# Kernel optimization log

Hardware: AMD Instinct MI355X
Metric: run time of the kernel (lower is better)

## Reference

```python
import jax, jax.numpy as jnp
import numpy as np

# ---- static physical configuration (matches init_kwargs param dict) ----
NX = NY = 513
NL = 3
N_ENS = 4
LX = LY = 5120.0e3
DX = LX / (NX - 1)
DY = LY / (NY - 1)
F0 = 9.375e-5
BETA = 1.754e-11
A2 = 0.0
A4 = 2.0e9
DELTA_EK = 2.0
TAU0 = 2.0e-5
BCCO = 0.2
ZFBC = BCCO / (1.0 + 0.5 * BCCO)
DT = 600.0
NUM_STEPS = 4
HEIGHTS = np.array([350.0, 750.0, 2900.0])
RED_G = np.array([0.025, 0.0125])

JAC_COEF = 1.0 / (F0 * DX * DY)
HYPERDIFF_COEF = A4 / F0**2 / DX**6
BOTTOM_FRICTION_COEF = DELTA_EK / (2.0 * abs(F0) * DX**2 * (-HEIGHTS[-1]))


def _build_constants():
    """Precompute stratification / mode / Helmholtz matrices (float64 numpy, cast to f32)."""
    A = np.zeros((NL, NL))
    A[0, 0] = 1.0 / (HEIGHTS[0] * RED_G[0])
    A[0, 1] = -1.0 / (HEIGHTS[0] * RED_G[0])
    for i in range(1, NL - 1):
        A[i, i - 1] = -1.0 / (HEIGHTS[i] * RED_G[i - 1])
        A[i, i] = 1.0 / HEIGHTS[i] * (1.0 / RED_G[i] + 1.0 / RED_G[i - 1])
        A[i, i + 1] = -1.0 / (HEIGHTS[i] * RED_G[i])
    A[-1, -1] = 1.0 / (HEIGHTS[NL - 1] * RED_G[NL - 2])
    A[-1, -2] = -1.0 / (HEIGHTS[NL - 1] * RED_G[NL - 2])
    lam_r, R = np.linalg.eig(A)
    lam_l, L = np.linalg.eig(A.T)
    lam_r, R, lam_l, L = lam_r.real, R.real, lam_l.real, L.real
    # align left eigenvectors with right eigenvalue ordering (biorthogonality)
    order = np.array([int(np.argmin(np.abs(lam_l - lr))) for lr in lam_r])
    L = L[:, order]
    Cl2m = np.diag(1.0 / np.diag(L.T @ R)) @ L.T
    Cm2l = R
    lambd = lam_r
    # DST-I eigenvalues of the 5-point Laplacian on the interior grid
    xg, yg = np.meshgrid(np.arange(1, NX - 1), np.arange(1, NY - 1), indexing='ij')
    lap_dst = (2 * (np.cos(np.pi / (NX - 1) * xg) - 1) / DX**2
               + 2 * (np.cos(np.pi / (NY - 1) * yg) - 1) / DY**2)
    helm_dst = lap_dst[None] / F0**2 - lambd[:, None, None]  # (nl, nx-2, ny-2)

    def np_dstI1D(x):
        N = x.shape[-1]
        xp = np.zeros(x.shape[:-1] + (N + 2,))
        xp[..., 1:-1] = x
        return np.fft.irfft(-1j * xp, n=2 * (N + 1), axis=-1, norm='ortho')[..., 1:N + 1]

    def np_dstI2D(x):
        return np.swapaxes(np_dstI1D(np.swapaxes(np_dstI1D(x), -1, -2)), -1, -2)

    const = np.ones((NL, NX, NY)) / (NX * NY)
    s = np.zeros_like(const)
    s[:, 1:-1, 1:-1] = np_dstI2D(np_dstI2D(const[:, 1:-1, 1:-1]) / helm_dst)
    hom_sol = (const + s * lambd[:, None, None])[:-1]  # (nl-1, nx, ny)
    M = (Cm2l[1:] - Cm2l[:-1])[:NL - 1, :NL - 1] * hom_sol.mean((1, 2))[None, :]
    alpha = -np.linalg.inv(M) @ (Cm2l[1:, :-1] - Cm2l[:-1, :-1])
    # wind forcing: curl(tau)/(f0*H1) on interior points; tau_y = 0, tau_x(y) only
    tau_x = -TAU0 * np.cos(2 * np.pi * (np.arange(NY) + 0.5) / NY)[None, :] * np.ones((NX, NY))
    dtaux_dy = (tau_x[1:-1, 2:] - tau_x[1:-1, :-2]) / (2 * DY)
    wind = (-dtaux_dy / (F0 * HEIGHTS[0]))[None]  # (1, nx-2, ny-2)
    f32 = lambda a: jnp.asarray(a, jnp.float32)
    return dict(A=f32(A), Cl2m=f32(Cl2m), Cm2l=f32(Cm2l), helmoltz_dst=f32(helm_dst),
                alpha_matrix=f32(alpha), homogeneous_sol=f32(hom_sol), wind_forcing=f32(wind))


# ---------------- stencil ops ----------------

def _pad11(x):
    return jnp.pad(x, [(0, 0)] * (x.ndim - 2) + [(1, 1), (1, 1)])


def laplacian_h_nobc(f):
    # unscaled 5-point Laplacian, interior values only: (..., nx-2, ny-2)
    return (f[..., 2:, 1:-1] + f[..., :-2, 1:-1] + f[..., 1:-1, 2:] + f[..., 1:-1, :-2]
            - 4.0 * f[..., 1:-1, 1:-1])


def laplacian_h(f, fc):
    # full-grid Laplacian with partial-slip boundary treatment (coefficient fc = zfbc)
    lap = _pad11(laplacian_h_nobc(f))
    lap = lap.at[..., 0, :].set(fc * (f[..., 1, :] - f[..., 0, :]))
    lap = lap.at[..., -1, :].set(fc * (f[..., -2, :] - f[..., -1, :]))
    lap = lap.at[..., :, 0].set(fc * (f[..., :, 1] - f[..., :, 0]))
    lap = lap.at[..., :, -1].set(fc * (f[..., :, -2] - f[..., :, -1]))
    return lap


def laplacian_h_boundaries(f, fc):
    # boundary Laplacian values, concat order: x=0 (y interior), x=-1, y=0 (full x), y=-1
    return jnp.concatenate([
        fc * (f[..., 1, 1:-1] - f[..., 0, 1:-1]),
        fc * (f[..., -2, 1:-1] - f[..., -1, 1:-1]),
        fc * (f[..., :, 1] - f[..., :, 0]),
        fc * (f[..., :, -2] - f[..., :, -1])], axis=-1)


def jacobi_h(f, g):
    # Arakawa 9-point Jacobian J(f, g), interior values (..., nx-2, ny-2)
    dx_f = f[..., 2:, :] - f[..., :-2, :]
    dx_g = g[..., 2:, :] - g[..., :-2, :]
    dy_f = f[..., 2:] - f[..., :-2]
    dy_g = g[..., 2:] - g[..., :-2]
    return ((dx_f[..., 1:-1] * dy_g[..., 1:-1, :] - dx_g[..., 1:-1] * dy_f[..., 1:-1, :])
            + (f[..., 2:, 1:-1] * dy_g[..., 2:, :] - f[..., :-2, 1:-1] * dy_g[..., :-2, :])
            - (f[..., 1:-1, 2:] * dx_g[..., 2:] - f[..., 1:-1, :-2] * dx_g[..., :-2])
            + (g[..., 1:-1, 2:] * dx_f[..., 2:] - g[..., 1:-1, :-2] * dx_f[..., :-2])
            - (g[..., 2:, 1:-1] * dy_f[..., 2:, :] - g[..., :-2, 1:-1] * dy_f[..., :-2, :])) / 12.0


# ---------------- DST-I elliptic solve ----------------

def dstI1D(x):
    N = x.shape[-1]
    z = jnp.zeros(x.shape[:-1] + (1,), x.dtype)
    xp = jnp.concatenate([z, x, z], axis=-1)
    return jnp.fft.irfft(-1j * xp.astype(jnp.complex64), n=2 * (N + 1), axis=-1,
                         norm='ortho')[..., 1:N + 1]


def dstI2D(x):
    return jnp.swapaxes(dstI1D(jnp.swapaxes(dstI1D(x), -1, -2)), -1, -2)


def inverse_elliptic_dst(f, op_dst):
    return dstI2D(dstI2D(f) / op_dst)


# ---------------- QG time derivative ----------------

def _time_derivatives(y, A, Cl2m, Cm2l, helm_dst, alpha, hom_sol, wind):
    q, p = y[0], y[1]  # (..., nl, nx, ny)
    # advection + hyperdiffusion RHS on interior (a_2 == 0 branch skipped as in source)
    rhs = JAC_COEF * jacobi_h(q, p)
    delta2_p = laplacian_h(p, ZFBC)
    rhs = rhs - HYPERDIFF_COEF * laplacian_h_nobc(laplacian_h(delta2_p, ZFBC))
    rhs = rhs.at[..., 0:1, :, :].add(wind)
    rhs = rhs.at[..., -1:, :, :].add(BOTTOM_FRICTION_COEF * laplacian_h_nobc(p[..., -1:, :, :]))
    dq = _pad11(rhs)
    # layers -> modes, DST Helmholtz inversion, homogeneous-solution correction
    rhs_h = jnp.einsum('ij,...jxy->...ixy', Cl2m, dq)
    dp_modes = _pad11(inverse_elliptic_dst(rhs_h[..., 1:-1, 1:-1], helm_dst))
    mean_m = dp_modes[..., :-1, :, :].mean((-2, -1))  # (..., nl-1)
    dalpha = jnp.einsum('ij,...j->...i', alpha, mean_m)[..., None, None]
    dp_modes = dp_modes.at[..., :-1, :, :].add(dalpha * hom_sol)
    dp = jnp.einsum('ij,...jxy->...ixy', Cm2l, dp_modes)
    # boundary vorticity update
    dp_bound = jnp.concatenate([dp[..., 0, 1:-1], dp[..., -1, 1:-1],
                                dp[..., :, 0], dp[..., :, -1]], axis=-1)
    delta_p_bound = laplacian_h_boundaries(dp / (F0 * DX)**2, ZFBC)
    dq_bound = delta_p_bound - jnp.einsum('ij,...jl->...il', A, dp_bound)
    ny2 = NY - 2
    dq = dq.at[..., 0, 1:-1].set(dq_bound[..., :ny2])
    dq = dq.at[..., -1, 1:-1].set(dq_bound[..., ny2:2 * ny2])
    dq = dq.at[..., :, 0].set(dq_bound[..., 2 * ny2:2 * ny2 + NX])
    dq = dq.at[..., :, -1].set(dq_bound[..., 2 * ny2 + NX:2 * ny2 + 2 * NX])
    return jnp.stack((dq, dp), 0)


def _forecast(y0, t, A, Cl2m, Cm2l, helm_dst, alpha, hom_sol, wind):
    deriv = lambda y: _time_derivatives(y, A, Cl2m, Cm2l, helm_dst, alpha, hom_sol, wind)

    def step(y, dt_):
        k1 = deriv(y)
        k2 = deriv(y + 0.5 * dt_ * k1)
        k3 = deriv(y + 0.5 * dt_ * k2)
        k4 = deriv(y + dt_ * k3)
        y_next = y + (dt_ / 6.0) * (k1 + 2.0 * k2 + 2.0 * k3 + k4)
        return y_next, y_next

    _, traj = jax.lax.scan(step, y0, t[1:] - t[:-1])
    return jnp.concatenate([y0[None], traj], axis=0)  # (T, 2, n_ens, nl, nx, ny)


def setup_inputs() -> dict:
    key = jax.random.key(0)
    y0 = 0.1 * jax.random.normal(key, (2, N_ENS, NL, NX, NY), dtype=jnp.float32)
    t = jnp.arange(NUM_STEPS + 1, dtype=jnp.float32) * DT
    consts = _build_constants()
    return dict(y0=y0, t=t, **consts)


def reference(y0, t, A, Cl2m, Cm2l, helmoltz_dst, alpha_matrix, homogeneous_sol, wind_forcing):
    return _forecast(y0, t, A, Cl2m, Cm2l, helmoltz_dst, alpha_matrix,
                     homogeneous_sol, wind_forcing)
```

## Files before the change

### kernel.cpp

```cpp
#include <hip/hip_runtime.h>
#include <math.h>

#define NXY 513
#define NIN 511
#define NL3 3
#define NE4 4
#define NB 12
#define GLD 512

static constexpr long FS  = (long)NE4 * NL3 * NXY * NXY;
static constexpr long GSZ = (long)NB * GLD * GLD;
static constexpr int  NSTEPS = 4;

static constexpr double dF0 = 9.375e-05;
static constexpr double dDX = 10000.0;
static constexpr float ZFBCf     = (float)(0.2 / (1.0 + 0.5 * 0.2));
static constexpr float JACCf     = (float)(1.0 / (dF0 * dDX * dDX));
static constexpr float HYPCf     = (float)(2.0e9 / (dF0 * dF0) / (dDX*dDX*dDX*dDX*dDX*dDX));
static constexpr float BFCf      = (float)(2.0 / (2.0 * dF0 * dDX * dDX * (-2900.0)));
static constexpr float INVF0DX2f = (float)(1.0 / ((dF0 * dDX) * (dF0 * dDX)));

typedef short  bf16x8 __attribute__((ext_vector_type(8)));
typedef float  f32x4  __attribute__((ext_vector_type(4)));
typedef unsigned int u32;
typedef __attribute__((address_space(1))) const u32 GAS;
typedef __attribute__((address_space(3))) u32 LAS;
#define GLDS(gp, lp) __builtin_amdgcn_global_load_lds((GAS*)(gp), (LAS*)(lp), 16, 0, 0)

__device__ __forceinline__ unsigned short f2bf(float x) {
    unsigned int u = __float_as_uint(x);
    return (unsigned short)((u + 0x7FFFu + ((u >> 16) & 1u)) >> 16);
}
__device__ __forceinline__ float bf2f(unsigned short h) {
    return __uint_as_float(((unsigned int)h) << 16);
}

__global__ void initB_kernel(unsigned short* __restrict__ BoH, unsigned short* __restrict__ BoL,
                             unsigned short* __restrict__ BeH, unsigned short* __restrict__ BeL) {
    int j = threadIdx.x;
    int n = blockIdx.x;
    int idx = n * 256 + j;
    int mo = ((n + 1) * (2 * j + 1)) & 1023;
    int me = ((n + 1) * (2 * j + 2)) & 1023;
    float fo = (float)(0.0625 * sin(M_PI * (double)mo / 512.0));
    float fe = (float)(0.0625 * sin(M_PI * (double)me / 512.0));
    unsigned short oh = f2bf(fo);
    BoH[idx] = oh; BoL[idx] = f2bf(fo - bf2f(oh));
    unsigned short eh = f2bf(fe);
    BeH[idx] = eh; BeL[idx] = f2bf(fe - bf2f(eh));
}

__global__ __launch_bounds__(256) void fused_rhs(
    float* __restrict__ kq, const float* __restrict__ q, const float* __restrict__ p,
    const float* __restrict__ wind)
{
    __shared__ float ps[22][72];
    __shared__ float qs[22][72];
    __shared__ float l1[22][72];
    __shared__ float l2[22][72];
    const int c  = blockIdx.z;
    const int x0 = 1 + blockIdx.y * 16;
    const int y0 = 1 + blockIdx.x * 64;
    const int t  = threadIdx.x;
    const size_t off = (size_t)c * NXY * NXY;
    const float* pp = p + off;
    const float* qp = q + off;

    for (int idx = t; idx < 22 * 70; idx += 256) {
        int i = idx / 70, j = idx % 70;
        int gx = x0 - 3 + i, gy = y0 - 3 + j;
        bool in = (gx >= 0 && gx < NXY && gy >= 0 && gy < NXY);
        size_t go = (size_t)gx * NXY + gy;
        ps[i][j] = in ? pp[go] : 0.f;
        qs[i][j] = in ? qp[go] : 0.f;
    }
    __syncthreads();

#define LAPBC(a, i, j, gx, gy) \
    ((gy) == 0       ? ZFBCf * (a[i][(j)+1] - a[i][j]) : \
     (gy) == NXY-1   ? ZFBCf * (a[i][(j)-1] - a[i][j]) : \
     (gx) == 0       ? ZFBCf * (a[(i)+1][j] - a[i][j]) : \
     (gx) == NXY-1   ? ZFBCf * (a[(i)-1][j] - a[i][j]) : \
     a[(i)+1][j] + a[(i)-1][j] + a[i][(j)+1] + a[i][(j)-1] - 4.f * a[i][j])

    for (int idx = t; idx < 20 * 68; idx += 256) {
        int i = 1 + idx / 68, j = 1 + idx % 68;
        int gx = x0 - 3 + i, gy = y0 - 3 + j;
        float v = 0.f;
        if (gx >= 0 && gx < NXY && gy >= 0 && gy < NXY) v = LAPBC(ps, i, j, gx, gy);
        l1[i][j] = v;
    }
    __syncthreads();

    for (int idx = t; idx < 18 * 66; idx += 256) {
        int i = 2 + idx / 66, j = 2 + idx % 66;
        int gx = x0 - 3 + i, gy = y0 - 3 + j;
        float v = 0.f;
        if (gx >= 0 && gx < NXY && gy >= 0 && gy < NXY) v = LAPBC(l1, i, j, gx, gy);
        l2[i][j] = v;
    }
    __syncthreads();
#undef LAPBC

    const int l = c % NL3;
    for (int idx = t; idx < 16 * 64; idx += 256) {
        int i = 3 + idx / 64, j = 3 + idx % 64;
        int gx = x0 - 3 + i, gy = y0 - 3 + j;
        if (gx > NIN || gy > NIN) continue;
        float fmm=qs[i-1][j-1], fm0=qs[i-1][j], fmp=qs[i-1][j+1];
        float f0m=qs[i][j-1],                    f0p=qs[i][j+1];
        float fpm=qs[i+1][j-1], fp0=qs[i+1][j], fpp=qs[i+1][j+1];
        float gmm=ps[i-1][j-1], gm0=ps[i-1][j], gmp=ps[i-1][j+1];
        float g0m=ps[i][j-1],   g00=ps[i][j],   g0p=ps[i][j+1];
        float gpm=ps[i+1][j-1], gp0=ps[i+1][j], gpp=ps[i+1][j+1];
        float J1 = (fp0 - fm0) * (g0p - g0m) - (gp0 - gm0) * (f0p - f0m);
        float J2 = fp0 * (gpp - gpm) - fm0 * (gmp - gmm);
        float J3 = f0p * (gpp - gmp) - f0m * (gpm - gmm);
        float J4 = g0p * (fpp - fmp) - g0m * (fpm - fmm);
        float J5 = gp0 * (fpp - fpm) - gm0 * (fmp - fmm);
        float jac = (J1 + J2 - J3 + J4 - J5) * (1.0f / 12.0f);
        float lap3 = l2[i+1][j] + l2[i-1][j] + l2[i][j+1] + l2[i][j-1] - 4.f * l2[i][j];
        float v = JACCf * jac - HYPCf * lap3;
        if (l == 0)       v += wind[(size_t)(gx-1) * NIN + (gy-1)];
        if (l == NL3-1)   v += BFCf * (gp0 + gm0 + g0p + g0m - 4.f * g00);
        kq[off + (size_t)gx * NXY + gy] = v;
    }
}

__global__ void l2m_kernel(unsigned short* __restrict__ Gh, unsigned short* __restrict__ Gl,
                           const float* __restrict__ kq, const float* __restrict__ Cl2m) {
    int p  = blockIdx.x * blockDim.x + threadIdx.x;
    int rx = blockIdx.y * blockDim.y + threadIdx.y;
    int e = blockIdx.z;
    int ry0 = 2 * p, ry1 = 2 * p + 1;
    float vA[3] = {0.f, 0.f, 0.f}, vB[3] = {0.f, 0.f, 0.f};
    if (rx < NIN) {
        size_t base = ((size_t)(e * NL3) * NXY + (rx + 1)) * NXY;
        if (ry0 < NIN) {
            float f0 = kq[base + ry0 + 1];
            float f1 = kq[base + (size_t)NXY*NXY + ry0 + 1];
            float f2 = kq[base + 2*(size_t)NXY*NXY + ry0 + 1];
            vA[0] = Cl2m[0]*f0 + Cl2m[1]*f1 + Cl2m[2]*f2;
            vA[1] = Cl2m[3]*f0 + Cl2m[4]*f1 + Cl2m[5]*f2;
            vA[2] = Cl2m[6]*f0 + Cl2m[7]*f1 + Cl2m[8]*f2;
        }
        if (ry1 < NIN) {
            float f0 = kq[base + ry1 + 1];
            float f1 = kq[base + (size_t)NXY*NXY + ry1 + 1];
            float f2 = kq[base + 2*(size_t)NXY*NXY + ry1 + 1];
            vB[0] = Cl2m[0]*f0 + Cl2m[1]*f1 + Cl2m[2]*f2;
            vB[1] = Cl2m[3]*f0 + Cl2m[4]*f1 + Cl2m[5]*f2;
            vB[2] = Cl2m[6]*f0 + Cl2m[7]*f1 + Cl2m[8]*f2;
        }
    }
#pragma unroll
    for (int i = 0; i < 3; ++i) {
        size_t pb = (size_t)(e * NL3 + i) * 262144;
        size_t po = pb + (size_t)rx * 256 + p;
        size_t pe = po + 131072;
        unsigned short ha = f2bf(vA[i]);
        Gh[po] = ha; Gl[po] = f2bf(vA[i] - bf2f(ha));
        unsigned short hb = f2bf(vB[i]);
        Gh[pe] = hb; Gl[pe] = f2bf(vB[i] - bf2f(hb));
    }
}

#define EPLD 68
__global__ __launch_bounds__(256, 3) void gemm_dst(
    const unsigned short* __restrict__ Ah, const unsigned short* __restrict__ Al,
    const unsigned short* __restrict__ BoH, const unsigned short* __restrict__ BoL,
    const unsigned short* __restrict__ BeH, const unsigned short* __restrict__ BeL,
    unsigned short* __restrict__ Ch, unsigned short* __restrict__ Cl,
    float* __restrict__ Cf, const float* __restrict__ helm)
{
    __shared__ __attribute__((aligned(16))) char lds[49152];
    float* ep1 = (float*)lds;
    float* ep2 = ep1 + 32 * EPLD;
    const int id = blockIdx.x;
    const int nblk = id / 96, rr = id - nblk * 96;
    const int b = rr >> 3, mblk = rr & 7;
    const int m0 = mblk << 6;
    const int n0t = nblk << 5;
    const int t = threadIdx.x;
    const int w = t >> 6, lane = t & 63;
    const int wn = w >> 1, wm = w & 1;
    const int lr = lane & 15, g = lane >> 4;
    const unsigned short* AbH = Ah + (size_t)b * 262144;
    const unsigned short* AbL = Al + (size_t)b * 262144;

    const int srA = t >> 2;
    const int scA = ((t & 3) ^ ((srA >> 1) & 3)) * 8;
    const size_t gA = (size_t)(m0 + srA) * 256 + scA;
    const int dA = t * 16;
    const int hid = t & 127;
    const int srB = hid >> 2;
    const int scB = ((hid & 3) ^ ((srB >> 1) & 3)) * 8;
    const size_t gB = (size_t)(n0t + srB) * 256 + scB;
    const unsigned short* B1 = (t < 128) ? BoH : BoL;
    const unsigned short* B2 = (t < 128) ? BeH : BeL;
    const int dB1 = ((t < 128) ? 16384 : 18432) + hid * 16;
    const int dB2 = ((t < 128) ? 20480 : 22528) + hid * 16;

    auto STAGE = [&](int buf, int kt) {
        char* bb = lds + buf * 24576;
        int ke = kt * 32;
        GLDS(AbH + gA + ke,          bb + dA);
        GLDS(AbL + gA + ke,          bb + 4096  + dA);
        GLDS(AbH + 131072 + gA + ke, bb + 8192  + dA);
        GLDS(AbL + 131072 + gA + ke, bb + 12288 + dA);
        GLDS(B1 + gB + ke, bb + dB1);
        GLDS(B2 + gB + ke, bb + dB2);
    };

    f32x4 accO[2] = {}, accE[2] = {};
    int abyte[2];
#pragma unroll
    for (int i = 0; i < 2; ++i) {
        int ar = wm*32 + i*16 + lr;
        abyte[i] = ar*64 + ((g ^ ((ar >> 1) & 3)) * 16);
    }
    const int brl = wn*16 + lr;
    const int bby = brl*64 + ((g ^ ((brl >> 1) & 3)) * 16);

    STAGE(0, 0);
    __syncthreads();
    for (int it = 0; it < 8; ++it) {
        const int buf = it & 1;
        if (it < 7) STAGE(buf ^ 1, it + 1);
        const char* bb = lds + buf * 24576;
        bf16x8 boH = *(const bf16x8*)(bb + 16384 + bby);
        bf16x8 boL = *(const bf16x8*)(bb + 18432 + bby);
        bf16x8 beH = *(const bf16x8*)(bb + 20480 + bby);
        bf16x8 beL = *(const bf16x8*)(bb + 22528 + bby);
#pragma unroll
        for (int i = 0; i < 2; ++i) {
            bf16x8 aoH = *(const bf16x8*)(bb + abyte[i]);
            bf16x8 aoL = *(const bf16x8*)(bb + 4096  + abyte[i]);
            bf16x8 aeH = *(const bf16x8*)(bb + 8192  + abyte[i]);
            bf16x8 aeL = *(const bf16x8*)(bb + 12288 + abyte[i]);
            accO[i] = __builtin_amdgcn_mfma_f32_16x16x32_bf16(aoH, boH, accO[i], 0, 0, 0);
            accO[i] = __builtin_amdgcn_mfma_f32_16x16x32_bf16(aoH, boL, accO[i], 0, 0, 0);
            accO[i] = __builtin_amdgcn_mfma_f32_16x16x32_bf16(aoL, boH, accO[i], 0, 0, 0);
            accE[i] = __builtin_amdgcn_mfma_f32_16x16x32_bf16(aeH, beH, accE[i], 0, 0, 0);
            accE[i] = __builtin_amdgcn_mfma_f32_16x16x32_bf16(aeH, beL, accE[i], 0, 0, 0);
            accE[i] = __builtin_amdgcn_mfma_f32_16x16x32_bf16(aeL, beH, accE[i], 0, 0, 0);
        }
        __syncthreads();
    }

    const int mode = b % NL3;
    const float* hp = helm ? (helm + (size_t)mode * NIN * NIN) : nullptr;
    const int nl = wn*16 + lr;
    const int r1g = n0t + nl;
    const int r2g = 510 - n0t - nl;
#pragma unroll
    for (int i = 0; i < 2; ++i) {
        int ml = wm*32 + i*16 + 4*g;
#pragma unroll
        for (int r = 0; r < 4; ++r) {
            float o = accO[i][r], e = accE[i][r];
            float v1 = o + e, v2 = o - e;
            int mg = m0 + ml + r;
            if (hp && mg < NIN) {
                v1 /= hp[(size_t)r1g * NIN + mg];
                v2 /= hp[(size_t)r2g * NIN + mg];
            }
            ep1[nl*EPLD + ml + r] = v1;
            ep2[nl*EPLD + ml + r] = v2;
        }
    }
    __syncthreads();

    {
        const int row = t >> 3;
        const int cb = (t & 7) * 8;
        const int r1 = n0t + row;
        const int r2 = 510 - n0t - row;
        float v1[8], v2[8];
#pragma unroll
        for (int k = 0; k < 8; ++k) { v1[k] = ep1[row*EPLD + cb + k]; v2[k] = ep2[row*EPLD + cb + k]; }
        if (Cf) {
            size_t c1 = (size_t)b*262144 + (size_t)r1*512 + m0 + cb;
            size_t c2 = (size_t)b*262144 + (size_t)r2*512 + m0 + cb;
            f32x4 a0 = {v1[0], v1[1], v1[2], v1[3]};
            f32x4 a1 = {v1[4], v1[5], v1[6], v1[7]};
            f32x4 b0 = {v2[0], v2[1], v2[2], v2[3]};
            f32x4 b1 = {v2[4], v2[5], v2[6], v2[7]};
            *(f32x4*)(Cf + c1) = a0; *(f32x4*)(Cf + c1 + 4) = a1;
            *(f32x4*)(Cf + c2) = b0; *(f32x4*)(Cf + c2 + 4) = b1;
            if (nblk == 0 && t < 64) Cf[(size_t)b*262144 + (size_t)511*512 + m0 + t] = 0.f;
        } else {
            auto STROW = [&](int rrow, const float* v) {
                size_t po = (size_t)b*262144 + (size_t)rrow*256 + ((m0 + cb) >> 1);
                size_t pe = po + 131072;
                unsigned short eh[4], el[4], oh[4], ol[4];
#pragma unroll
                for (int k = 0; k < 4; ++k) {
                    float ve = v[2*k], vo = v[2*k+1];
                    eh[k] = f2bf(ve); el[k] = f2bf(ve - bf2f(eh[k]));
                    oh[k] = f2bf(vo); ol[k] = f2bf(vo - bf2f(oh[k]));
                }
                *(uint2*)(Ch + po) = make_uint2((u32)eh[0] | ((u32)eh[1] << 16), (u32)eh[2] | ((u32)eh[3] << 16));
                *(uint2*)(Cl + po) = make_uint2((u32)el[0] | ((u32)el[1] << 16), (u32)el[2] | ((u32)el[3] << 16));
                *(uint2*)(Ch + pe) = make_uint2((u32)oh[0] | ((u32)oh[1] << 16), (u32)oh[2] | ((u32)oh[3] << 16));
                *(uint2*)(Cl + pe) = make_uint2((u32)ol[0] | ((u32)ol[1] << 16), (u32)ol[2] | ((u32)ol[3] << 16));
            };
            STROW(r1, v1);
            STROW(r2, v2);
            if (nblk == 0 && t < 32) {
                size_t z = (size_t)b*262144 + (size_t)511*256 + (m0 >> 1) + t;
                Ch[z] = 0; Cl[z] = 0; Ch[z + 131072] = 0; Cl[z + 131072] = 0;
            }
        }
    }
}

__global__ void mean_kernel(float* __restrict__ partial, const float* __restrict__ G) {
    int gy = blockIdx.y;
    int e = gy >> 1, m = gy & 1;
    const float* g = G + (size_t)(e * NL3 + m) * GLD * GLD;
    float s = 0.f;
    for (int idx = blockIdx.x * 256 + threadIdx.x; idx < GLD*GLD; idx += 64 * 256)
        s += g[idx];
    __shared__ float red[256];
    red[threadIdx.x] = s; __syncthreads();
    for (int w = 128; w >= 1; w >>= 1) {
        if (threadIdx.x < w) red[threadIdx.x] += red[threadIdx.x + w];
        __syncthreads();
    }
    if (threadIdx.x == 0) partial[gy * 64 + blockIdx.x] = red[0];
}

__global__ void dalpha_kernel(float* __restrict__ dal, const float* __restrict__ partial,
                              const float* __restrict__ alpha) {
    int t = threadIdx.x;
    if (t >= 8) return;
    int e = t >> 1, i = t & 1;
    float s0 = 0.f, s1 = 0.f;
    for (int bk = 0; bk < 64; ++bk) { s0 += partial[(e*2+0)*64 + bk]; s1 += partial[(e*2+1)*64 + bk]; }
    const float inv = 1.0f / ((float)NXY * (float)NXY);
    dal[t] = alpha[i*2+0] * (s0 * inv) + alpha[i*2+1] * (s1 * inv);
}

__global__ void m2l_kernel(float* __restrict__ kp, const float* __restrict__ G,
                           const float* __restrict__ dal, const float* __restrict__ hom,
                           const float* __restrict__ Cm2l) {
    int y = blockIdx.x * blockDim.x + threadIdx.x;
    int x = blockIdx.y * blockDim.y + threadIdx.y;
    int e = blockIdx.z;
    if (x >= NXY || y >= NXY) return;
    float mv[3];
    bool interior = (x >= 1 && x <= NIN && y >= 1 && y <= NIN);
#pragma unroll
    for (int i = 0; i < 3; ++i)
        mv[i] = interior ? G[(size_t)(e*NL3 + i) * GLD * GLD + (size_t)(x-1) * GLD + (y-1)] : 0.f;
    float h0 = hom[(size_t)x * NXY + y];
    float h1 = hom[(size_t)NXY*NXY + (size_t)x * NXY + y];
    mv[0] += dal[e*2 + 0] * h0;
    mv[1] += dal[e*2 + 1] * h1;
#pragma unroll
    for (int l = 0; l < 3; ++l)
        kp[((size_t)(e*NL3 + l) * NXY + x) * NXY + y] =
            Cm2l[l*3+0]*mv[0] + Cm2l[l*3+1]*mv[1] + Cm2l[l*3+2]*mv[2];
}

__global__ void bound_kernel(float* __restrict__ kq, const float* __restrict__ kp,
                             const float* __restrict__ Amat) {
    int pos = blockIdx.x * 256 + threadIdx.x;
    int e = blockIdx.y;
    if (pos >= 2048) return;
    int x, y, xn, yn;
    if (pos < NIN)            { x = 0;      y = pos + 1;        xn = 1;      yn = y; }
    else if (pos < 2*NIN)     { x = NXY-1;  y = pos - NIN + 1;  xn = NXY-2;  yn = y; }
    else if (pos < 2*NIN+NXY) { x = pos - 2*NIN;       y = 0;      xn = x; yn = 1; }
    else                      { x = pos - (2*NIN+NXY); y = NXY-1;  xn = x; yn = NXY-2; }
    float dpb[3], lpb[3];
#pragma unroll
    for (int j = 0; j < 3; ++j) {
        const float* f = kp + (size_t)(e*NL3 + j) * NXY * NXY;
        float c = f[(size_t)x * NXY + y];
        float nb = f[(size_t)xn * NXY + yn];
        dpb[j] = c;
        lpb[j] = ZFBCf * INVF0DX2f * (nb - c);
    }
#pragma unroll
    for (int l = 0; l < 3; ++l) {
        float v = lpb[l] - (Amat[l*3+0]*dpb[0] + Amat[l*3+1]*dpb[1] + Amat[l*3+2]*dpb[2]);
        kq[((size_t)(e*NL3 + l) * NXY + x) * NXY + y] = v;
    }
}

__global__ void rk_fused(float4* __restrict__ o1, float4* __restrict__ o2,
                         const float4* __restrict__ x, const float4* __restrict__ k,
                         float c1, float c2, int accumulate,
                         const float* __restrict__ t, int s, long n4) {
    float dt = t[s+1] - t[s];
    float a1 = c1 * dt, a2 = c2 * dt;
    for (long i = (long)blockIdx.x * blockDim.x + threadIdx.x; i < n4;
         i += (long)gridDim.x * blockDim.x) {
        float4 kk = k[i], xx = x[i];
        float4 b0 = accumulate ? o1[i] : xx;
        o1[i] = make_float4(b0.x + a1*kk.x, b0.y + a1*kk.y, b0.z + a1*kk.z, b0.w + a1*kk.w);
        if (o2) o2[i] = make_float4(xx.x + a2*kk.x, xx.y + a2*kk.y, xx.z + a2*kk.z, xx.w + a2*kk.w);
    }
}

__global__ void copy_kernel(float4* __restrict__ out, const float4* __restrict__ in, long n4) {
    for (long i = (long)blockIdx.x * blockDim.x + threadIdx.x; i < n4;
         i += (long)gridDim.x * blockDim.x)
        out[i] = in[i];
}

extern "C" void kernel_launch(void* const* d_in, const int* in_sizes, int n_in,
                              void* d_out, int out_size, void* d_ws, size_t ws_size,
                              hipStream_t stream) {
    const float* y0    = (const float*)d_in[0];
    const float* tarr  = (const float*)d_in[1];
    const float* Amat  = (const float*)d_in[2];
    const float* Cl2m  = (const float*)d_in[3];
    const float* Cm2l  = (const float*)d_in[4];
    const float* helm  = (const float*)d_in[5];
    const float* alpha = (const float*)d_in[6];
    const float* hom   = (const float*)d_in[7];
    const float* wind  = (const float*)d_in[8];
    float* out = (float*)d_out;
    char* base = (char*)d_ws;

    unsigned short* BoH = (unsigned short*)base;
    unsigned short* BoL = BoH + 65536;
    unsigned short* BeH = BoL + 65536;
    unsigned short* BeL = BeH + 65536;
    float* ytmp = (float*)(base + 1024*1024);
    float* kbuf = ytmp + 2*FS;
    char*  REGb = (char*)(kbuf + 2*FS);
    unsigned short* P0h = (unsigned short*)REGb;
    unsigned short* P0l = P0h + GSZ;
    unsigned short* P1h = P0l + GSZ;
    unsigned short* P1l = P1h + GSZ;
    float* R4 = (float*)REGb;
    float* partial = (float*)(REGb + (size_t)2*FS*sizeof(float));
    float* dal = partial + 512;

    const dim3 bSt(64, 4, 1);
    const dim3 gSt4((NXY + 63)/64, (NXY + 3)/4, NE4);
    const dim3 gL2M(4, 128, NE4);
    const dim3 gF(8, 32, NB);
    const dim3 gG(768, 1, 1);
    const long n4 = 2*FS/4;

    initB_kernel<<<256, 256, 0, stream>>>(BoH, BoL, BeH, BeL);
    copy_kernel<<<1024, 256, 0, stream>>>((float4*)out, (const float4*)y0, n4);

    auto deriv = [&](const float* y, float* k) {
        const float* q = y;  const float* p = y + FS;
        float* kq = k;       float* kp = k + FS;
        fused_rhs<<<gF, 256, 0, stream>>>(kq, q, p, wind);
        l2m_kernel<<<gL2M, bSt, 0, stream>>>(P0h, P0l, kq, Cl2m);
        gemm_dst<<<gG, 256, 0, stream>>>(P0h, P0l, BoH, BoL, BeH, BeL, P1h, P1l, nullptr, nullptr);
        gemm_dst<<<gG, 256, 0, stream>>>(P1h, P1l, BoH, BoL, BeH, BeL, P0h, P0l, nullptr, helm);
        gemm_dst<<<gG, 256, 0, stream>>>(P0h, P0l, BoH, BoL, BeH, BeL, P1h, P1l, nullptr, nullptr);
        gemm_dst<<<gG, 256, 0, stream>>>(P1h, P1l, BoH, BoL, BeH, BeL, nullptr, nullptr, R4, nullptr);
        mean_kernel<<<dim3(64, 8), 256, 0, stream>>>(partial, R4);
        dalpha_kernel<<<1, 64, 0, stream>>>(dal, partial, alpha);
        m2l_kernel<<<gSt4, bSt, 0, stream>>>(kp, R4, dal, hom, Cm2l);
        bound_kernel<<<dim3(8, NE4), 256, 0, stream>>>(kq, kp, Amat);
    };

    for (int s = 0; s < NSTEPS; ++s) {
        float* ycur  = out + (size_t)s * 2 * FS;
        float* ynext = out + (size_t)(s + 1) * 2 * FS;
        deriv(ycur, kbuf);
        rk_fused<<<1024, 256, 0, stream>>>((float4*)ynext, (float4*)ytmp, (const float4*)ycur,
                                           (const float4*)kbuf, 1.f/6.f, 0.5f, 0, tarr, s, n4);
        deriv(ytmp, kbuf);
        rk_fused<<<1024, 256, 0, stream>>>((float4*)ynext, (float4*)ytmp, (const float4*)ycur,
                                           (const float4*)kbuf, 2.f/6.f, 0.5f, 1, tarr, s, n4);
        deriv(ytmp, kbuf);
        rk_fused<<<1024, 256, 0, stream>>>((float4*)ynext, (float4*)ytmp, (const float4*)ycur,
                                           (const float4*)kbuf, 2.f/6.f, 1.0f, 1, tarr, s, n4);
        deriv(ytmp, kbuf);
        rk_fused<<<1024, 256, 0, stream>>>((float4*)ynext, nullptr, (const float4*)ycur,
                                           (const float4*)kbuf, 1.f/6.f, 0.f, 1, tarr, s, n4);
    }
}
```

Baseline: 2.147 ms.

## Fuse mean reduction into final DST GEMM and merge m2l, dalpha, boundary kernels

The last DST GEMM now computes per-block partial sums of its float output in the epilogue. This removes the separate mean_kernel pass that re-read the whole result buffer. The dalpha, mode-to-layer and boundary kernels are merged into one m2l_bound kernel: each block reduces the partials itself and boundary threads recompute their neighbour values instead of re-reading kp. This cuts three launches and one full-field read per derivative evaluation. In exchange it adds an LDS tree reduction and extra syncs to the GEMM, and every m2l block redundantly reduces 128 partials.

```diff
diff --git a/kernel.cpp b/kernel.cpp
--- a/kernel.cpp
+++ b/kernel.cpp
@@ -171,9 +171,10 @@
     const unsigned short* __restrict__ BoH, const unsigned short* __restrict__ BoL,
     const unsigned short* __restrict__ BeH, const unsigned short* __restrict__ BeL,
     unsigned short* __restrict__ Ch, unsigned short* __restrict__ Cl,
-    float* __restrict__ Cf, const float* __restrict__ helm)
+    float* __restrict__ Cf, const float* __restrict__ helm, float* __restrict__ part)
 {
     __shared__ __attribute__((aligned(16))) char lds[49152];
+    __shared__ float red[256];
     float* ep1 = (float*)lds;
     float* ep2 = ep1 + 32 * EPLD;
     const int id = blockIdx.x;
@@ -271,6 +272,7 @@
     }
     __syncthreads();
 
+    float lsum = 0.f;
     {
         const int row = t >> 3;
         const int cb = (t & 7) * 8;
@@ -289,6 +291,12 @@
             *(f32x4*)(Cf + c1) = a0; *(f32x4*)(Cf + c1 + 4) = a1;
             *(f32x4*)(Cf + c2) = b0; *(f32x4*)(Cf + c2 + 4) = b1;
             if (nblk == 0 && t < 64) Cf[(size_t)b*262144 + (size_t)511*512 + m0 + t] = 0.f;
+#pragma unroll
+            for (int k = 0; k < 8; ++k) lsum += v1[k];
+            if (r1 != 255) {
+#pragma unroll
+                for (int k = 0; k < 8; ++k) lsum += v2[k];
+            }
         } else {
             auto STROW = [&](int rrow, const float* v) {
                 size_t po = (size_t)b*262144 + (size_t)rrow*256 + ((m0 + cb) >> 1);
@@ -313,80 +321,84 @@
             }
         }
     }
-}
-
-__global__ void mean_kernel(float* __restrict__ partial, const float* __restrict__ G) {
-    int gy = blockIdx.y;
-    int e = gy >> 1, m = gy & 1;
-    const float* g = G + (size_t)(e * NL3 + m) * GLD * GLD;
-    float s = 0.f;
-    for (int idx = blockIdx.x * 256 + threadIdx.x; idx < GLD*GLD; idx += 64 * 256)
-        s += g[idx];
-    __shared__ float red[256];
-    red[threadIdx.x] = s; __syncthreads();
-    for (int w = 128; w >= 1; w >>= 1) {
-        if (threadIdx.x < w) red[threadIdx.x] += red[threadIdx.x + w];
+
+    if (part && Cf && mode < 2) {
         __syncthreads();
-    }
-    if (threadIdx.x == 0) partial[gy * 64 + blockIdx.x] = red[0];
-}
-
-__global__ void dalpha_kernel(float* __restrict__ dal, const float* __restrict__ partial,
-                              const float* __restrict__ alpha) {
-    int t = threadIdx.x;
-    if (t >= 8) return;
-    int e = t >> 1, i = t & 1;
-    float s0 = 0.f, s1 = 0.f;
-    for (int bk = 0; bk < 64; ++bk) { s0 += partial[(e*2+0)*64 + bk]; s1 += partial[(e*2+1)*64 + bk]; }
-    const float inv = 1.0f / ((float)NXY * (float)NXY);
-    dal[t] = alpha[i*2+0] * (s0 * inv) + alpha[i*2+1] * (s1 * inv);
-}
-
-__global__ void m2l_kernel(float* __restrict__ kp, const float* __restrict__ G,
-                           const float* __restrict__ dal, const float* __restrict__ hom,
-                           const float* __restrict__ Cm2l) {
-    int y = blockIdx.x * blockDim.x + threadIdx.x;
-    int x = blockIdx.y * blockDim.y + threadIdx.y;
-    int e = blockIdx.z;
-    if (x >= NXY || y >= NXY) return;
-    float mv[3];
-    bool interior = (x >= 1 && x <= NIN && y >= 1 && y <= NIN);
-#pragma unroll
-    for (int i = 0; i < 3; ++i)
-        mv[i] = interior ? G[(size_t)(e*NL3 + i) * GLD * GLD + (size_t)(x-1) * GLD + (y-1)] : 0.f;
-    float h0 = hom[(size_t)x * NXY + y];
-    float h1 = hom[(size_t)NXY*NXY + (size_t)x * NXY + y];
-    mv[0] += dal[e*2 + 0] * h0;
-    mv[1] += dal[e*2 + 1] * h1;
+        red[t] = lsum;
+        __syncthreads();
+        for (int w2 = 128; w2 >= 1; w2 >>= 1) {
+            if (t < w2) red[t] += red[t + w2];
+            __syncthreads();
+        }
+        if (t == 0) {
+            int plane8 = (b / NL3) * 2 + mode;
+            part[plane8 * 64 + nblk * 8 + mblk] = red[0];
+        }
+    }
+}
+
+__global__ __launch_bounds__(256) void m2l_bound(
+    float* __restrict__ kp, float* __restrict__ kq,
+    const float* __restrict__ G, const float* __restrict__ hom,
+    const float* __restrict__ Cm2l, const float* __restrict__ Amat,
+    const float* __restrict__ alpha, const float* __restrict__ part)
+{
+    __shared__ float sp[128];
+    __shared__ float sdal[2];
+    const int yy = blockIdx.x * 64 + threadIdx.x;
+    const int xx = blockIdx.y * 4 + threadIdx.y;
+    const int e  = blockIdx.z;
+    const int tt = threadIdx.y * 64 + threadIdx.x;
+
+    if (tt < 128) sp[tt] = part[(e*2 + (tt >> 6))*64 + (tt & 63)];
+    __syncthreads();
+    if (tt == 0) {
+        float s0 = 0.f, s1 = 0.f;
+        for (int j = 0; j < 64; ++j) { s0 += sp[j]; s1 += sp[64 + j]; }
+        const float inv = 1.0f / ((float)NXY * (float)NXY);
+        float mm0 = s0 * inv, mm1 = s1 * inv;
+        sdal[0] = alpha[0]*mm0 + alpha[1]*mm1;
+        sdal[1] = alpha[2]*mm0 + alpha[3]*mm1;
+    }
+    __syncthreads();
+    if (xx >= NXY || yy >= NXY) return;
+    const float dal0 = sdal[0], dal1 = sdal[1];
+
+    auto DP = [&](int px, int py, float* dp) {
+        bool inter = (px >= 1 && px <= NIN && py >= 1 && py <= NIN);
+        float mv0 = 0.f, mv1 = 0.f, mv2 = 0.f;
+        if (inter) {
+            size_t gb = (size_t)(e*NL3)*GLD*GLD + (size_t)(px-1)*GLD + (py-1);
+            mv0 = G[gb]; mv1 = G[gb + (size_t)GLD*GLD]; mv2 = G[gb + 2*(size_t)GLD*GLD];
+        }
+        mv0 += dal0 * hom[(size_t)px*NXY + py];
+        mv1 += dal1 * hom[(size_t)NXY*NXY + (size_t)px*NXY + py];
+        dp[0] = Cm2l[0]*mv0 + Cm2l[1]*mv1 + Cm2l[2]*mv2;
+        dp[1] = Cm2l[3]*mv0 + Cm2l[4]*mv1 + Cm2l[5]*mv2;
+        dp[2] = Cm2l[6]*mv0 + Cm2l[7]*mv1 + Cm2l[8]*mv2;
+    };
+
+    float dp[3];
+    DP(xx, yy, dp);
 #pragma unroll
     for (int l = 0; l < 3; ++l)
-        kp[((size_t)(e*NL3 + l) * NXY + x) * NXY + y] =
-            Cm2l[l*3+0]*mv[0] + Cm2l[l*3+1]*mv[1] + Cm2l[l*3+2]*mv[2];
-}
-
-__global__ void bound_kernel(float* __restrict__ kq, const float* __restrict__ kp,
-                             const float* __restrict__ Amat) {
-    int pos = blockIdx.x * 256 + threadIdx.x;
-    int e = blockIdx.y;
-    if (pos >= 2048) return;
-    int x, y, xn, yn;
-    if (pos < NIN)            { x = 0;      y = pos + 1;        xn = 1;      yn = y; }
-    else if (pos < 2*NIN)     { x = NXY-1;  y = pos - NIN + 1;  xn = NXY-2;  yn = y; }
-    else if (pos < 2*NIN+NXY) { x = pos - 2*NIN;       y = 0;      xn = x; yn = 1; }
-    else                      { x = pos - (2*NIN+NXY); y = NXY-1;  xn = x; yn = NXY-2; }
-    float dpb[3], lpb[3];
-#pragma unroll
-    for (int j = 0; j < 3; ++j) {
-        const float* f = kp + (size_t)(e*NL3 + j) * NXY * NXY;
-        float c = f[(size_t)x * NXY + y];
-        float nb = f[(size_t)xn * NXY + yn];
-        dpb[j] = c;
-        lpb[j] = ZFBCf * INVF0DX2f * (nb - c);
-    }
-#pragma unroll
-    for (int l = 0; l < 3; ++l) {
-        float v = lpb[l] - (Amat[l*3+0]*dpb[0] + Amat[l*3+1]*dpb[1] + Amat[l*3+2]*dpb[2]);
-        kq[((size_t)(e*NL3 + l) * NXY + x) * NXY + y] = v;
+        kp[((size_t)(e*NL3 + l)*NXY + xx)*NXY + yy] = dp[l];
+
+    const bool bnd = (xx == 0 || xx == NXY-1 || yy == 0 || yy == NXY-1);
+    if (bnd) {
+        int xn, yn;
+        if      (yy == 0)      { xn = xx;    yn = 1; }
+        else if (yy == NXY-1)  { xn = xx;    yn = NXY-2; }
+        else if (xx == 0)      { xn = 1;     yn = yy; }
+        else                   { xn = NXY-2; yn = yy; }
+        float dpn[3];
+        DP(xn, yn, dpn);
+#pragma unroll
+        for (int l = 0; l < 3; ++l) {
+            float lpb = ZFBCf * INVF0DX2f * (dpn[l] - dp[l]);
+            kq[((size_t)(e*NL3 + l)*NXY + xx)*NXY + yy] =
+                lpb - (Amat[l*3+0]*dp[0] + Amat[l*3+1]*dp[1] + Amat[l*3+2]*dp[2]);
+        }
     }
 }
 
@@ -439,7 +451,6 @@
     unsigned short* P1l = P1h + GSZ;
     float* R4 = (float*)REGb;
     float* partial = (float*)(REGb + (size_t)2*FS*sizeof(float));
-    float* dal = partial + 512;
 
     const dim3 bSt(64, 4, 1);
     const dim3 gSt4((NXY + 63)/64, (NXY + 3)/4, NE4);
@@ -456,14 +467,11 @@
         float* kq = k;       float* kp = k + FS;
         fused_rhs<<<gF, 256, 0, stream>>>(kq, q, p, wind);
         l2m_kernel<<<gL2M, bSt, 0, stream>>>(P0h, P0l, kq, Cl2m);
-        gemm_dst<<<gG, 256, 0, stream>>>(P0h, P0l, BoH, BoL, BeH, BeL, P1h, P1l, nullptr, nullptr);
-        gemm_dst<<<gG, 256, 0, stream>>>(P1h, P1l, BoH, BoL, BeH, BeL, P0h, P0l, nullptr, helm);
-        gemm_dst<<<gG, 256, 0, stream>>>(P0h, P0l, BoH, BoL, BeH, BeL, P1h, P1l, nullptr, nullptr);
-        gemm_dst<<<gG, 256, 0, stream>>>(P1h, P1l, BoH, BoL, BeH, BeL, nullptr, nullptr, R4, nullptr);
-        mean_kernel<<<dim3(64, 8), 256, 0, stream>>>(partial, R4);
-        dalpha_kernel<<<1, 64, 0, stream>>>(dal, partial, alpha);
-        m2l_kernel<<<gSt4, bSt, 0, stream>>>(kp, R4, dal, hom, Cm2l);
-        bound_kernel<<<dim3(8, NE4), 256, 0, stream>>>(kq, kp, Amat);
+        gemm_dst<<<gG, 256, 0, stream>>>(P0h, P0l, BoH, BoL, BeH, BeL, P1h, P1l, nullptr, nullptr, nullptr);
+        gemm_dst<<<gG, 256, 0, stream>>>(P1h, P1l, BoH, BoL, BeH, BeL, P0h, P0l, nullptr, helm, nullptr);
+        gemm_dst<<<gG, 256, 0, stream>>>(P0h, P0l, BoH, BoL, BeH, BeL, P1h, P1l, nullptr, nullptr, nullptr);
+        gemm_dst<<<gG, 256, 0, stream>>>(P1h, P1l, BoH, BoL, BeH, BeL, nullptr, nullptr, R4, nullptr, partial);
+        m2l_bound<<<gSt4, bSt, 0, stream>>>(kp, kq, R4, hom, Cm2l, Amat, alpha, partial);
     };
 
     for (int s = 0; s < NSTEPS; ++s) {
```

Result: faster. 2.008 ms (median of 3 runs) (-6.5%).
